# Kernel optimization log

Measured on AMD Instinct MI355X. Metric: run time of the kernel, lower is better.

The kernel has to match this reference:

```python
import jax, jax.numpy as jnp
import numpy as np

STATE_LEN = 128

def _layernorm(x, eps=1e-5):
    m = jnp.mean(x, axis=-1, keepdims=True)
    v = jnp.mean(jnp.square(x - m), axis=-1, keepdims=True)
    return (x - m) * jax.lax.rsqrt(v + eps)

def setup_inputs() -> dict:
    key = jax.random.key(0)
    ks = jax.random.split(key, 20)
    B, S, L = 2, 2048, STATE_LEN
    Din, Dk, Dv, H = 1024, 64, 64, 8
    T = S + 2 * L  # 2304
    x = jax.random.normal(ks[0], (B, T, Din), jnp.float32)
    def w(k, dout):
        return jax.random.normal(k, (H, Din, dout), jnp.float32) / np.sqrt(Din).astype(np.float32)
    inp = {
        'x': x,
        'ln_g':  1.0 + 0.02 * jax.random.normal(ks[1], (H, Din), jnp.float32),
        'ln_b':  0.02 * jax.random.normal(ks[2], (H, Din), jnp.float32),
        'ln_gs': 1.0 + 0.02 * jax.random.normal(ks[3], (H, Din), jnp.float32),
        'ln_bs': 0.02 * jax.random.normal(ks[4], (H, Din), jnp.float32),
        'ln_ge': 1.0 + 0.02 * jax.random.normal(ks[5], (H, Din), jnp.float32),
        'ln_be': 0.02 * jax.random.normal(ks[6], (H, Din), jnp.float32),
        'Wq':   w(ks[7], Dk),  'Wk':   w(ks[8], Dk),  'Wv':   w(ks[9], Dv),
        'Wq_s': w(ks[10], Dk), 'Wk_s': w(ks[11], Dk), 'Wv_s': w(ks[12], Dv),
        'Wq_e': w(ks[13], Dk), 'Wk_e': w(ks[14], Dk), 'Wv_e': w(ks[15], Dv),
        'offset': 0,
    }
    return inp

def _forward(x, ln_g, ln_b, ln_gs, ln_bs, ln_ge, ln_be,
             Wq, Wk, Wv, Wq_s, Wk_s, Wv_s, Wq_e, Wk_e, Wv_e):
    L = STATE_LEN
    B, T, Din = x.shape
    # extract_state: start state, middle sequence, end state
    xs, xm, xe = x[:, :L], x[:, L:T - L], x[:, T - L:]
    # LayerNorm stats are parameter-free; per-head affine applied after
    ns, nm, ne = _layernorm(xs), _layernorm(xm), _layernorm(xe)
    def aff(n, g, b):  # [B,seg,Din] -> [B,H,seg,Din]
        return n[:, None, :, :] * g[None, :, None, :] + b[None, :, None, :]
    hs, hm, he = aff(ns, ln_gs, ln_bs), aff(nm, ln_g, ln_b), aff(ne, ln_ge, ln_be)
    proj = lambda h, W: jnp.einsum('bhsd,hde->bhse', h, W)
    q = jnp.concatenate([proj(hs, Wq_s), proj(hm, Wq), proj(he, Wq_e)], axis=2)
    k = jnp.concatenate([proj(hs, Wk_s), proj(hm, Wk), proj(he, Wk_e)], axis=2)
    v = jnp.concatenate([proj(hs, Wv_s), proj(hm, Wv), proj(he, Wv_e)], axis=2)
    Dk = q.shape[-1]
    scores = jnp.einsum('bhsd,bhtd->bhst', q, k) / jnp.asarray(np.sqrt(Dk), q.dtype)
    # Faithful to the torch code: a FLOAT tril-of-ones mask is passed to SDPA,
    # which ADDS it to the scores (it does not set -inf anywhere).
    mask = jnp.tril(jnp.ones((T, T), scores.dtype))
    att = jax.nn.softmax(scores + mask, axis=-1)
    out = jnp.einsum('bhst,bhtd->bhsd', att, v)  # [B,H,T,Dv]
    H, Dv = out.shape[1], out.shape[3]
    # torch.concat over heads on last dim
    return out.transpose(0, 2, 1, 3).reshape(B, T, H * Dv)

def reference(x, ln_g, ln_b, ln_gs, ln_bs, ln_ge, ln_be,
              Wq, Wk, Wv, Wq_s, Wk_s, Wv_s, Wq_e, Wk_e, Wv_e, offset):
    # offset unused: position_embedders are None in this configuration
    return _forward(x, ln_g, ln_b, ln_gs, ln_bs, ln_ge, ln_be,
                    Wq, Wk, Wv, Wq_s, Wk_s, Wv_s, Wq_e, Wk_e, Wv_e)
```

## Files before the change

kernel.cpp:

```cpp
#include <hip/hip_runtime.h>

#define TSEQ 2304
#define DIN  1024
#define NH   8
#define DD   64
#define NC   1536
#define MROWS 4608
#define L2E  1.44269504f
#define EF   2.71828183f

typedef __attribute__((ext_vector_type(8))) short bf16x8;
typedef __attribute__((ext_vector_type(4))) float f32x4;
typedef __attribute__((ext_vector_type(16))) float f32x16;
typedef __attribute__((ext_vector_type(4))) unsigned short u16x4;
typedef __attribute__((ext_vector_type(4))) unsigned int u32x4;

__device__ __forceinline__ unsigned short f2bf(float f){
    union { float f; unsigned int u; } x; x.f = f;
    unsigned int r = x.u + 0x7FFFu + ((x.u >> 16) & 1u);
    return (unsigned short)(r >> 16);
}

__device__ __forceinline__ float exp2raw(float x){
    float r;
    asm("v_exp_f32 %0, %1" : "=v"(r) : "v"(x));
    return r;
}

__device__ __forceinline__ unsigned int cvtpk(float a, float b){
    unsigned int r;
    asm("v_cvt_pk_bf16_f32 %0, %1, %2" : "=v"(r) : "v"(a), "v"(b));
    return r;
}

__device__ __forceinline__ void gload_lds16(const void* g, void* l){
    __builtin_amdgcn_global_load_lds(
        (const __attribute__((address_space(1))) void*)g,
        (__attribute__((address_space(3))) void*)l, 16, 0, 0);
}

struct WArgs {
    const float* W[9];
    const float* g[3];
    const float* bv[3];
};

__global__ __launch_bounds__(256) void k_pre(WArgs a, const float* __restrict__ x,
                                             unsigned short* __restrict__ wb,
                                             float* __restrict__ bias,
                                             unsigned short* __restrict__ nrm)
{
    __shared__ float lds[64][65];
    __shared__ float red[4][64];
    __shared__ float r1[4], r2[4];
    const int bid = blockIdx.x;
    const int tid = threadIdx.x;
    if (bid < 1152){
        const int dt = bid & 15, h = (bid >> 4) & 7, sp = bid >> 7;
        const int seg = sp / 3, proj = sp % 3;
        const float* W = a.W[seg*3 + proj];
        const float* g = a.g[seg];
        const int d0 = dt * 64;
        {
            const int e = tid & 63, rq = tid >> 6;
#pragma unroll
            for (int rr = 0; rr < 16; ++rr){
                const int dl = rr*4 + rq;
                lds[dl][e] = W[((size_t)h*DIN + d0 + dl)*DD + e];
            }
        }
        __syncthreads();
        {
            const int dl = tid & 63, eq = tid >> 6;
            const int n0 = proj*512 + h*64;
            const float gv = g[h*DIN + d0 + dl];
#pragma unroll
            for (int rr = 0; rr < 16; ++rr){
                const int el = eq*16 + rr;
                wb[((size_t)seg*NC + n0 + el)*DIN + d0 + dl] = f2bf(lds[dl][el] * gv);
            }
        }
    } else if (bid < 1224){
        const int u = bid - 1152;
        const int h = u & 7, sp = u >> 3;
        const int seg = sp / 3, proj = sp % 3;
        const float* W  = a.W[seg*3 + proj];
        const float* bv = a.bv[seg];
        const int e = tid & 63, dc = tid >> 6;
        float sum = 0.f;
        for (int i = 0; i < 256; ++i){
            const int d = dc*256 + i;
            sum += bv[h*DIN + d] * W[((size_t)h*DIN + d)*DD + e];
        }
        red[dc][e] = sum;
        __syncthreads();
        if (dc == 0)
            bias[seg*NC + proj*512 + h*64 + e] = red[0][e] + red[1][e] + red[2][e] + red[3][e];
    } else {
        const int row = bid - 1224;
        const float* xr = x + (size_t)row * DIN;
        f32x4 v = *(const f32x4*)&xr[tid*4];
        float s1 = v[0]+v[1]+v[2]+v[3];
        float s2 = v[0]*v[0]+v[1]*v[1]+v[2]*v[2]+v[3]*v[3];
#pragma unroll
        for (int m = 1; m < 64; m <<= 1){ s1 += __shfl_xor(s1, m); s2 += __shfl_xor(s2, m); }
        const int wid = tid >> 6;
        if ((tid & 63) == 0){ r1[wid] = s1; r2[wid] = s2; }
        __syncthreads();
        s1 = r1[0]+r1[1]+r1[2]+r1[3];
        s2 = r2[0]+r2[1]+r2[2]+r2[3];
        const float mean = s1 * (1.f/1024.f);
        const float var  = s2 * (1.f/1024.f) - mean*mean;
        const float rstd = rsqrtf(var + 1e-5f);
        u16x4 ov;
#pragma unroll
        for (int j = 0; j < 4; ++j) ov[j] = f2bf((v[j]-mean)*rstd);
        *(u16x4*)&nrm[(size_t)row*DIN + tid*4] = ov;
    }
}

__global__ __launch_bounds__(256) void k_gemm(
    const unsigned short* __restrict__ A,
    const unsigned short* __restrict__ Wb,
    const float* __restrict__ bias,
    unsigned short* __restrict__ qo,
    unsigned short* __restrict__ ko,
    unsigned short* __restrict__ vt)
{
    __shared__ unsigned short As[128*64];
    __shared__ unsigned short Bs[128*64];
    const int mt = blockIdx.x, nt = blockIdx.y;
    const int row0 = mt*128, n0 = nt*128;
    const int rloc = row0 % TSEQ;
    const int seg = (rloc < 128) ? 0 : (rloc < 2176 ? 1 : 2);
    const unsigned short* Bp = Wb + (size_t)seg * NC * DIN;
    const int tid = threadIdx.x;
    const int wid = tid >> 6, lane = tid & 63;
    const int wr = wid >> 1, wc = wid & 1;
    const int lr = lane & 15, lg = lane >> 4;
    const int rsub = lane >> 3;
    const int cgx  = (lane & 7) ^ rsub;
    f32x4 acc[4][4];
#pragma unroll
    for (int m = 0; m < 4; ++m)
#pragma unroll
        for (int n = 0; n < 4; ++n) acc[m][n] = (f32x4){0.f,0.f,0.f,0.f};

    for (int kt = 0; kt < DIN/64; ++kt){
        const int k0 = kt*64;
        __syncthreads();
#pragma unroll
        for (int i = 0; i < 4; ++i){
            const int c = wid*4 + i;
            const int r = c*8 + rsub;
            gload_lds16(&A [(size_t)(row0 + r)*DIN + k0 + cgx*8], &As[c*512]);
            gload_lds16(&Bp[(size_t)(n0  + r)*DIN + k0 + cgx*8], &Bs[c*512]);
        }
        __syncthreads();
#pragma unroll
        for (int ks = 0; ks < 2; ++ks){
            bf16x8 af[4], bfr[4];
#pragma unroll
            for (int m = 0; m < 4; ++m)
                af[m]  = *(const bf16x8*)&As[(wr*64 + m*16 + lr)*64 + (((ks*4 + lg) ^ (lr & 7))*8)];
#pragma unroll
            for (int n = 0; n < 4; ++n)
                bfr[n] = *(const bf16x8*)&Bs[(wc*64 + n*16 + lr)*64 + (((ks*4 + lg) ^ (lr & 7))*8)];
#pragma unroll
            for (int m = 0; m < 4; ++m)
#pragma unroll
                for (int n = 0; n < 4; ++n)
                    acc[m][n] = __builtin_amdgcn_mfma_f32_16x16x32_bf16(af[m], bfr[n], acc[m][n], 0, 0, 0);
        }
    }
    const int b_ = row0 / TSEQ;
    const int t0 = row0 - b_ * TSEQ;
#pragma unroll
    for (int m = 0; m < 4; ++m){
#pragma unroll
        for (int n = 0; n < 4; ++n){
            const int nglob = n0 + wc*64 + n*16 + lr;
            const float bs = bias[seg*NC + nglob];
            const int proj = nglob >> 9, hh = (nglob >> 6) & 7, e = nglob & 63;
            if (proj < 2){
                unsigned short* op = (proj == 0) ? qo : ko;
                const float scale = (proj == 0) ? 0.125f * L2E : 1.0f;
                const size_t ob = ((size_t)(b_*NH + hh) * TSEQ) * DD + e;
#pragma unroll
                for (int j = 0; j < 4; ++j){
                    const int t = t0 + wr*64 + m*16 + 4*lg + j;
                    op[ob + (size_t)t * DD] = f2bf((acc[m][n][j] + bs) * scale);
                }
            } else {
                unsigned short* vp = vt + ((size_t)(b_*NH + hh)*DD + e)*TSEQ;
                const int t = t0 + wr*64 + m*16 + 4*lg;
                u16x4 pk;
#pragma unroll
                for (int j = 0; j < 4; ++j) pk[j] = f2bf(acc[m][n][j] + bs);
                *(u16x4*)&vp[t] = pk;
            }
        }
    }
}

__global__ __launch_bounds__(256) void k_attn(
    const unsigned short* __restrict__ Q,
    const unsigned short* __restrict__ K,
    const unsigned short* __restrict__ Vt,
    float* __restrict__ po0,
    float* __restrict__ po1,
    float* __restrict__ out2,
    float* __restrict__ pl)
{
    __shared__ unsigned short Ks[2][64*64];
    __shared__ unsigned short Vs[2][64*64];
    const int qtb = blockIdx.x;
    const int bh  = blockIdx.y;
    const int z   = blockIdx.z;
    const int kt0 = z*12, kt1 = kt0 + 12;
    const int tid  = threadIdx.x;
    const int w    = tid >> 6;
    const int lane = tid & 63;
    const int l31  = lane & 31;
    const int h    = lane >> 5;
    const size_t qkb = (size_t)bh * TSEQ * DD;
    const size_t vtb = (size_t)bh * DD * TSEQ;
    const int q0w = qtb*128 + w*32;
    const int kd  = qtb*2 + (w >> 1);

    const int rsub = lane >> 3;
    const int cgx  = (lane & 7) ^ rsub;
    const char* Kbase  = (const char*)(K  + qkb);
    const char* Vtbase = (const char*)(Vt + vtb);

    bf16x8 aq[4];
#pragma unroll
    for (int ds = 0; ds < 4; ++ds)
        aq[ds] = *(const bf16x8*)&Q[qkb + (size_t)(q0w + l31)*DD + ds*16 + h*8];

    float lsum = 0.f;
    f32x16 o0, o1;
#pragma unroll
    for (int r = 0; r < 16; ++r){ o0[r] = 0.f; o1[r] = 0.f; }

    auto stage = [&](int kt, int b){
        const int kn = kt*64;
#pragma unroll
        for (int i = 0; i < 2; ++i){
            const int c = w*2 + i;
            const int r = c*8 + rsub;
            gload_lds16(Kbase  + (size_t)(kn + r)*128 + cgx*16,              &Ks[b][c*512]);
            gload_lds16(Vtbase + (size_t)r*(TSEQ*2) + (size_t)kn*2 + cgx*16, &Vs[b][c*512]);
        }
    };

    stage(kt0, 0);
    __syncthreads();

    const int rowA = l31 * 64;

    int buf = 0;
    for (int kt = kt0; kt < kt1; ++kt){
        const int kc0 = kt*64;
        if (kt + 1 < kt1) stage(kt + 1, buf ^ 1);
        f32x16 s0, s1;
#pragma unroll
        for (int r = 0; r < 16; ++r){ s0[r] = 0.f; s1[r] = 0.f; }
#pragma unroll
        for (int ds = 0; ds < 4; ++ds){
            const int sx = (((ds*2 + h) ^ (lane & 7)) * 8);
            bf16x8 kf0 = *(const bf16x8*)&Ks[buf][rowA + sx];
            bf16x8 kf1 = *(const bf16x8*)&Ks[buf][rowA + 2048 + sx];
            s0 = __builtin_amdgcn_mfma_f32_32x32x16_bf16(kf0, aq[ds], s0, 0, 0, 0);
            s1 = __builtin_amdgcn_mfma_f32_32x32x16_bf16(kf1, aq[ds], s1, 0, 0, 0);
        }
        if (kt == kd){
            lsum *= EF;
#pragma unroll
            for (int r = 0; r < 16; ++r){ o0[r] *= EF; o1[r] *= EF; }
            const int qr = q0w + l31;
#pragma unroll
            for (int r = 0; r < 16; ++r){
                const int kk = kc0 + (r&3) + 8*(r>>2) + 4*h;
                const float p0 = exp2raw(s0[r] + ((kk      <= qr) ? L2E : 0.f));
                const float p1 = exp2raw(s1[r] + ((kk + 32 <= qr) ? L2E : 0.f));
                s0[r] = p0; s1[r] = p1;
                lsum += p0 + p1;
            }
        } else {
#pragma unroll
            for (int r = 0; r < 16; ++r){
                const float p0 = exp2raw(s0[r]);
                const float p1 = exp2raw(s1[r]);
                s0[r] = p0; s1[r] = p1;
                lsum += p0 + p1;
            }
        }
#pragma unroll
        for (int ks = 0; ks < 4; ++ks){
            const int rb = (ks & 1) * 8;
            unsigned int a01, a23, b01, b23;
            if (ks < 2){
                a01 = cvtpk(s0[rb+0], s0[rb+1]); a23 = cvtpk(s0[rb+2], s0[rb+3]);
                b01 = cvtpk(s0[rb+4], s0[rb+5]); b23 = cvtpk(s0[rb+6], s0[rb+7]);
            } else {
                a01 = cvtpk(s1[rb+0], s1[rb+1]); a23 = cvtpk(s1[rb+2], s1[rb+3]);
                b01 = cvtpk(s1[rb+4], s1[rb+5]); b23 = cvtpk(s1[rb+6], s1[rb+7]);
            }
            asm("v_permlane32_swap_b32 %0, %1" : "+v"(a01), "+v"(b01));
            asm("v_permlane32_swap_b32 %0, %1" : "+v"(a23), "+v"(b23));
            u32x4 fw; fw[0] = a01; fw[1] = a23; fw[2] = b01; fw[3] = b23;
            bf16x8 pa = __builtin_bit_cast(bf16x8, fw);
            const int sx = (((ks*2 + h) ^ (lane & 7)) * 8);
            bf16x8 vf0 = *(const bf16x8*)&Vs[buf][rowA + sx];
            bf16x8 vf1 = *(const bf16x8*)&Vs[buf][rowA + 2048 + sx];
            o0 = __builtin_amdgcn_mfma_f32_32x32x16_bf16(pa, vf0, o0, 0, 0, 0);
            o1 = __builtin_amdgcn_mfma_f32_32x32x16_bf16(pa, vf1, o1, 0, 0, 0);
        }
        __syncthreads();
        buf ^= 1;
    }
    if (kd >= kt1){
        lsum *= EF;
#pragma unroll
        for (int r = 0; r < 16; ++r){ o0[r] *= EF; o1[r] *= EF; }
    }
    lsum += __shfl_xor(lsum, 32);
    const int pbase = ((z*16 + bh)*18 + qtb)*128 + w*32;
    if (h == 0) pl[pbase + l31] = lsum;
    if (z < 2){
        float* po = (z == 0) ? po0 : po1;
        const size_t tb = ((size_t)(bh*18 + qtb)*128 + w*32) * 64;
#pragma unroll
        for (int r = 0; r < 16; ++r){
            const int qloc = (r&3) + 8*(r>>2) + 4*h;
            po[tb + (size_t)qloc*64 + l31]      = o0[r];
            po[tb + (size_t)qloc*64 + 32 + l31] = o1[r];
        }
    } else {
        const int b_ = bh >> 3, hh = bh & 7;
#pragma unroll
        for (int r = 0; r < 16; ++r){
            const int qloc = (r&3) + 8*(r>>2) + 4*h;
            const size_t ob = ((size_t)(b_*TSEQ + q0w + qloc))*512 + hh*64;
            out2[ob + l31]      = o0[r];
            out2[ob + 32 + l31] = o1[r];
        }
    }
}

__global__ __launch_bounds__(256) void k_comb(
    const float* __restrict__ po0, const float* __restrict__ po1,
    const float* __restrict__ pl, float* __restrict__ out)
{
    const int qt = blockIdx.x, bh = blockIdx.y;
    const int b_ = bh >> 3, hh = bh & 7;
    const int tid = threadIdx.x;
    const int row = tid >> 2;
    const int c0  = (tid & 3) * 16;
    const int t128  = qt >> 1;
    const int rowin = (qt & 1)*64 + row;
    const int plb = (bh*18 + t128)*128 + rowin;
    const float inv = 1.0f / (pl[plb] + pl[(16*18*128) + plb] + pl[(2*16*18*128) + plb]);
    const size_t tb = ((size_t)(bh*18 + t128)*128 + rowin)*64 + c0;
    const size_t ob = ((size_t)(b_*TSEQ + qt*64 + row))*512 + hh*64 + c0;
#pragma unroll
    for (int i = 0; i < 4; ++i){
        f32x4 a = *(const f32x4*)&po0[tb + i*4];
        f32x4 b = *(const f32x4*)&po1[tb + i*4];
        f32x4 c = *(const f32x4*)&out[ob + i*4];
        f32x4 r;
#pragma unroll
        for (int j = 0; j < 4; ++j) r[j] = (a[j] + b[j] + c[j]) * inv;
        *(f32x4*)&out[ob + i*4] = r;
    }
}

extern "C" void kernel_launch(void* const* d_in, const int* in_sizes, int n_in,
                              void* d_out, int out_size, void* d_ws, size_t ws_size,
                              hipStream_t stream)
{
    const float* x     = (const float*)d_in[0];
    const float* ln_g  = (const float*)d_in[1];
    const float* ln_b  = (const float*)d_in[2];
    const float* ln_gs = (const float*)d_in[3];
    const float* ln_bs = (const float*)d_in[4];
    const float* ln_ge = (const float*)d_in[5];
    const float* ln_be = (const float*)d_in[6];
    const float* Wq    = (const float*)d_in[7];
    const float* Wk    = (const float*)d_in[8];
    const float* Wv    = (const float*)d_in[9];
    const float* Wq_s  = (const float*)d_in[10];
    const float* Wk_s  = (const float*)d_in[11];
    const float* Wv_s  = (const float*)d_in[12];
    const float* Wq_e  = (const float*)d_in[13];
    const float* Wk_e  = (const float*)d_in[14];
    const float* Wv_e  = (const float*)d_in[15];

    uint8_t* w = (uint8_t*)d_ws;
    unsigned short* nrm = (unsigned short*)(w);
    unsigned short* wb  = (unsigned short*)(w + 9437184);
    float*          bia = (float*)        (w + 18874368);
    unsigned short* q_  = (unsigned short*)(w + 18892800);
    unsigned short* k_  = (unsigned short*)(w + 23611392);
    unsigned short* vt_ = (unsigned short*)(w + 28329984);
    float*          pl  = (float*)        (w + 33048576);
    float*          po0 = (float*)        (w);
    float*          po1 = (float*)        (w + 9437184);

    WArgs wa;
    wa.W[0] = Wq_s; wa.W[1] = Wk_s; wa.W[2] = Wv_s;
    wa.W[3] = Wq;   wa.W[4] = Wk;   wa.W[5] = Wv;
    wa.W[6] = Wq_e; wa.W[7] = Wk_e; wa.W[8] = Wv_e;
    wa.g[0] = ln_gs; wa.g[1] = ln_g; wa.g[2] = ln_ge;
    wa.bv[0] = ln_bs; wa.bv[1] = ln_b; wa.bv[2] = ln_be;

    float* out = (float*)d_out;
    k_pre <<<dim3(5832),      dim3(256), 0, stream>>>(wa, x, wb, bia, nrm);
    k_gemm<<<dim3(36, 12),    dim3(256), 0, stream>>>(nrm, wb, bia, q_, k_, vt_);
    k_attn<<<dim3(18, 16, 3), dim3(256), 0, stream>>>(q_, k_, vt_, po0, po1, out, pl);
    k_comb<<<dim3(36, 16),    dim3(256), 0, stream>>>(po0, po1, pl, out);
}
```

Before: 97.61 us.

## Split keys across warps in attention block and reduce in LDS, drop combine kernel

```diff
diff --git a/kernel.cpp b/kernel.cpp
--- a/kernel.cpp
+++ b/kernel.cpp
@@ -207,17 +207,15 @@
     const unsigned short* __restrict__ Q,
     const unsigned short* __restrict__ K,
     const unsigned short* __restrict__ Vt,
-    float* __restrict__ po0,
-    float* __restrict__ po1,
-    float* __restrict__ out2,
-    float* __restrict__ pl)
+    float* __restrict__ out)
 {
-    __shared__ unsigned short Ks[2][64*64];
-    __shared__ unsigned short Vs[2][64*64];
-    const int qtb = blockIdx.x;
-    const int bh  = blockIdx.y;
-    const int z   = blockIdx.z;
-    const int kt0 = z*12, kt1 = kt0 + 12;
+    __shared__ float osum[4][32][64];
+    __shared__ float lsums[4][32];
+    const int bid = blockIdx.x;
+    const int bhLo = bid & 7;
+    const int rdec = bid >> 3;
+    const int qtb  = rdec % 72;
+    const int bh   = (rdec / 72) * 8 + bhLo;
     const int tid  = threadIdx.x;
     const int w    = tid >> 6;
     const int lane = tid & 63;
@@ -225,60 +223,49 @@
     const int h    = lane >> 5;
     const size_t qkb = (size_t)bh * TSEQ * DD;
     const size_t vtb = (size_t)bh * DD * TSEQ;
-    const int q0w = qtb*128 + w*32;
-    const int kd  = qtb*2 + (w >> 1);
-
-    const int rsub = lane >> 3;
-    const int cgx  = (lane & 7) ^ rsub;
-    const char* Kbase  = (const char*)(K  + qkb);
-    const char* Vtbase = (const char*)(Vt + vtb);
+    const int q0 = qtb * 32;
+    const int kd = qtb >> 1;
+    const int kt0 = w * 9, kt1 = kt0 + 9;
 
     bf16x8 aq[4];
 #pragma unroll
     for (int ds = 0; ds < 4; ++ds)
-        aq[ds] = *(const bf16x8*)&Q[qkb + (size_t)(q0w + l31)*DD + ds*16 + h*8];
+        aq[ds] = *(const bf16x8*)&Q[qkb + (size_t)(q0 + l31)*DD + ds*16 + h*8];
 
     float lsum = 0.f;
     f32x16 o0, o1;
 #pragma unroll
     for (int r = 0; r < 16; ++r){ o0[r] = 0.f; o1[r] = 0.f; }
 
-    auto stage = [&](int kt, int b){
-        const int kn = kt*64;
-#pragma unroll
-        for (int i = 0; i < 2; ++i){
-            const int c = w*2 + i;
-            const int r = c*8 + rsub;
-            gload_lds16(Kbase  + (size_t)(kn + r)*128 + cgx*16,              &Ks[b][c*512]);
-            gload_lds16(Vtbase + (size_t)r*(TSEQ*2) + (size_t)kn*2 + cgx*16, &Vs[b][c*512]);
-        }
-    };
-
-    stage(kt0, 0);
-    __syncthreads();
-
-    const int rowA = l31 * 64;
-
-    int buf = 0;
+    const unsigned short* Krow0 = K  + qkb + (size_t)l31 * DD;
+    const unsigned short* Vrow  = Vt + vtb + (size_t)l31 * TSEQ;
+
     for (int kt = kt0; kt < kt1; ++kt){
         const int kc0 = kt*64;
-        if (kt + 1 < kt1) stage(kt + 1, buf ^ 1);
+        bf16x8 kf0[4], kf1[4], vf0[4], vf1[4];
+#pragma unroll
+        for (int ds = 0; ds < 4; ++ds){
+            kf0[ds] = *(const bf16x8*)&Krow0[(size_t)(kc0)*DD      + ds*16 + h*8];
+            kf1[ds] = *(const bf16x8*)&Krow0[(size_t)(kc0 + 32)*DD + ds*16 + h*8];
+        }
+#pragma unroll
+        for (int ks = 0; ks < 4; ++ks){
+            vf0[ks] = *(const bf16x8*)&Vrow[kc0 + ks*16 + h*8];
+            vf1[ks] = *(const bf16x8*)&Vrow[(size_t)32*TSEQ + kc0 + ks*16 + h*8];
+        }
         f32x16 s0, s1;
 #pragma unroll
         for (int r = 0; r < 16; ++r){ s0[r] = 0.f; s1[r] = 0.f; }
 #pragma unroll
         for (int ds = 0; ds < 4; ++ds){
-            const int sx = (((ds*2 + h) ^ (lane & 7)) * 8);
-            bf16x8 kf0 = *(const bf16x8*)&Ks[buf][rowA + sx];
-            bf16x8 kf1 = *(const bf16x8*)&Ks[buf][rowA + 2048 + sx];
-            s0 = __builtin_amdgcn_mfma_f32_32x32x16_bf16(kf0, aq[ds], s0, 0, 0, 0);
-            s1 = __builtin_amdgcn_mfma_f32_32x32x16_bf16(kf1, aq[ds], s1, 0, 0, 0);
+            s0 = __builtin_amdgcn_mfma_f32_32x32x16_bf16(kf0[ds], aq[ds], s0, 0, 0, 0);
+            s1 = __builtin_amdgcn_mfma_f32_32x32x16_bf16(kf1[ds], aq[ds], s1, 0, 0, 0);
         }
         if (kt == kd){
             lsum *= EF;
 #pragma unroll
             for (int r = 0; r < 16; ++r){ o0[r] *= EF; o1[r] *= EF; }
-            const int qr = q0w + l31;
+            const int qr = q0 + l31;
 #pragma unroll
             for (int r = 0; r < 16; ++r){
                 const int kk = kc0 + (r&3) + 8*(r>>2) + 4*h;
@@ -311,14 +298,9 @@
             asm("v_permlane32_swap_b32 %0, %1" : "+v"(a23), "+v"(b23));
             u32x4 fw; fw[0] = a01; fw[1] = a23; fw[2] = b01; fw[3] = b23;
             bf16x8 pa = __builtin_bit_cast(bf16x8, fw);
-            const int sx = (((ks*2 + h) ^ (lane & 7)) * 8);
-            bf16x8 vf0 = *(const bf16x8*)&Vs[buf][rowA + sx];
-            bf16x8 vf1 = *(const bf16x8*)&Vs[buf][rowA + 2048 + sx];
-            o0 = __builtin_amdgcn_mfma_f32_32x32x16_bf16(pa, vf0, o0, 0, 0, 0);
-            o1 = __builtin_amdgcn_mfma_f32_32x32x16_bf16(pa, vf1, o1, 0, 0, 0);
-        }
-        __syncthreads();
-        buf ^= 1;
+            o0 = __builtin_amdgcn_mfma_f32_32x32x16_bf16(pa, vf0[ks], o0, 0, 0, 0);
+            o1 = __builtin_amdgcn_mfma_f32_32x32x16_bf16(pa, vf1[ks], o1, 0, 0, 0);
+        }
     }
     if (kd >= kt1){
         lsum *= EF;
@@ -326,53 +308,33 @@
         for (int r = 0; r < 16; ++r){ o0[r] *= EF; o1[r] *= EF; }
     }
     lsum += __shfl_xor(lsum, 32);
-    const int pbase = ((z*16 + bh)*18 + qtb)*128 + w*32;
-    if (h == 0) pl[pbase + l31] = lsum;
-    if (z < 2){
-        float* po = (z == 0) ? po0 : po1;
-        const size_t tb = ((size_t)(bh*18 + qtb)*128 + w*32) * 64;
-#pragma unroll
-        for (int r = 0; r < 16; ++r){
-            const int qloc = (r&3) + 8*(r>>2) + 4*h;
-            po[tb + (size_t)qloc*64 + l31]      = o0[r];
-            po[tb + (size_t)qloc*64 + 32 + l31] = o1[r];
-        }
-    } else {
+    if (h == 0) lsums[w][l31] = lsum;
+#pragma unroll
+    for (int r = 0; r < 16; ++r){
+        const int qloc = (r&3) + 8*(r>>2) + 4*h;
+        osum[w][qloc][l31]      = o0[r];
+        osum[w][qloc][l31 + 32] = o1[r];
+    }
+    __syncthreads();
+    {
+        const int q  = tid >> 3;
+        const int e0 = (tid & 7) * 8;
+        const float L = lsums[0][q] + lsums[1][q] + lsums[2][q] + lsums[3][q];
+        const float inv = 1.0f / L;
+        f32x4 r0 = (f32x4){0.f,0.f,0.f,0.f}, r1v = (f32x4){0.f,0.f,0.f,0.f};
+#pragma unroll
+        for (int ww = 0; ww < 4; ++ww){
+            f32x4 a = *(const f32x4*)&osum[ww][q][e0];
+            f32x4 b = *(const f32x4*)&osum[ww][q][e0 + 4];
+#pragma unroll
+            for (int j = 0; j < 4; ++j){ r0[j] += a[j]; r1v[j] += b[j]; }
+        }
+#pragma unroll
+        for (int j = 0; j < 4; ++j){ r0[j] *= inv; r1v[j] *= inv; }
         const int b_ = bh >> 3, hh = bh & 7;
-#pragma unroll
-        for (int r = 0; r < 16; ++r){
-            const int qloc = (r&3) + 8*(r>>2) + 4*h;
-            const size_t ob = ((size_t)(b_*TSEQ + q0w + qloc))*512 + hh*64;
-            out2[ob + l31]      = o0[r];
-            out2[ob + 32 + l31] = o1[r];
-        }
-    }
-}
-
-__global__ __launch_bounds__(256) void k_comb(
-    const float* __restrict__ po0, const float* __restrict__ po1,
-    const float* __restrict__ pl, float* __restrict__ out)
-{
-    const int qt = blockIdx.x, bh = blockIdx.y;
-    const int b_ = bh >> 3, hh = bh & 7;
-    const int tid = threadIdx.x;
-    const int row = tid >> 2;
-    const int c0  = (tid & 3) * 16;
-    const int t128  = qt >> 1;
-    const int rowin = (qt & 1)*64 + row;
-    const int plb = (bh*18 + t128)*128 + rowin;
-    const float inv = 1.0f / (pl[plb] + pl[(16*18*128) + plb] + pl[(2*16*18*128) + plb]);
-    const size_t tb = ((size_t)(bh*18 + t128)*128 + rowin)*64 + c0;
-    const size_t ob = ((size_t)(b_*TSEQ + qt*64 + row))*512 + hh*64 + c0;
-#pragma unroll
-    for (int i = 0; i < 4; ++i){
-        f32x4 a = *(const f32x4*)&po0[tb + i*4];
-        f32x4 b = *(const f32x4*)&po1[tb + i*4];
-        f32x4 c = *(const f32x4*)&out[ob + i*4];
-        f32x4 r;
-#pragma unroll
-        for (int j = 0; j < 4; ++j) r[j] = (a[j] + b[j] + c[j]) * inv;
-        *(f32x4*)&out[ob + i*4] = r;
+        const size_t ob = ((size_t)(b_*TSEQ + q0 + q))*512 + hh*64 + e0;
+        *(f32x4*)&out[ob]     = r0;
+        *(f32x4*)&out[ob + 4] = r1v;
     }
 }
 
@@ -404,9 +366,6 @@
     unsigned short* q_  = (unsigned short*)(w + 18892800);
     unsigned short* k_  = (unsigned short*)(w + 23611392);
     unsigned short* vt_ = (unsigned short*)(w + 28329984);
-    float*          pl  = (float*)        (w + 33048576);
-    float*          po0 = (float*)        (w);
-    float*          po1 = (float*)        (w + 9437184);
 
     WArgs wa;
     wa.W[0] = Wq_s; wa.W[1] = Wk_s; wa.W[2] = Wv_s;
@@ -416,8 +375,7 @@
     wa.bv[0] = ln_bs; wa.bv[1] = ln_b; wa.bv[2] = ln_be;
 
     float* out = (float*)d_out;
-    k_pre <<<dim3(5832),      dim3(256), 0, stream>>>(wa, x, wb, bia, nrm);
-    k_gemm<<<dim3(36, 12),    dim3(256), 0, stream>>>(nrm, wb, bia, q_, k_, vt_);
-    k_attn<<<dim3(18, 16, 3), dim3(256), 0, stream>>>(q_, k_, vt_, po0, po1, out, pl);
-    k_comb<<<dim3(36, 16),    dim3(256), 0, stream>>>(po0, po1, pl, out);
-}
+    k_pre <<<dim3(5832),   dim3(256), 0, stream>>>(wa, x, wb, bia, nrm);
+    k_gemm<<<dim3(36, 12), dim3(256), 0, stream>>>(nrm, wb, bia, q_, k_, vt_);
+    k_attn<<<dim3(1152),   dim3(256), 0, stream>>>(q_, k_, vt_, out);
+}
```

Result: slower. 130.4 us (+33.6%).
